# Kernel optimization log

Hardware: AMD Instinct MI355X
Metric: run time of the kernel (lower is better)

Reference implementation:

```python
import jax, jax.numpy as jnp
import numpy as np

B, I, O, N = 65536, 256, 32, 8


def chebyshev_basis(x, n):
    """Chebyshev polynomials T_0..T_{n-1} of x. x: [B, I] -> [B, I, n]."""
    T = [jnp.ones_like(x), x]
    for _ in range(n - 2):
        T.append(2.0 * x * T[-1] - T[-2])
    return jnp.stack(T[:n], axis=-1)


def setup_inputs() -> dict:
    key = jax.random.key(0)
    k1, k2 = jax.random.split(key)
    # inputs live on [-1, 1], the natural Chebyshev domain
    x = jax.random.uniform(k1, (B, I), jnp.float32, minval=-1.0, maxval=1.0)
    # weight init mirrors torch: uniform(-weight_magnitude/in, weight_magnitude/in)
    w = jax.random.uniform(k2, (O, I, N), jnp.float32, minval=-1.0 / I, maxval=1.0 / I)
    return {"x": x, "w": w}


def reference(x, w):
    n = w.shape[-1]
    phi = chebyshev_basis(x, n)          # [B, I, n] basis expansion
    out = jnp.einsum("bin,oin->bo", phi, w)  # weighted contraction
    return out
```

## Files before the change

### kernel.cpp

```cpp
#include <hip/hip_runtime.h>
#include <hip/hip_bf16.h>


typedef __attribute__((ext_vector_type(8)))  short bf16x8;
typedef __attribute__((ext_vector_type(16))) float f32x16;
typedef __attribute__((ext_vector_type(4)))  float f32x4;

__device__ __forceinline__ short f2b(float f) {
    __hip_bfloat16 h = __float2bfloat16(f);
    short s;
    __builtin_memcpy(&s, &h, sizeof(s));
    return s;
}

__device__ __forceinline__ unsigned pkbf_tr(float lo, float hi) {
    unsigned a, b;
    __builtin_memcpy(&a, &hi, 4);
    __builtin_memcpy(&b, &lo, 4);
    return __builtin_amdgcn_perm(a, b, 0x07060302u);
}

__global__ __launch_bounds__(256) void prep_w_kernel(const float* __restrict__ w,
                                                     short* __restrict__ wB) {
    int idx = blockIdx.x * 256 + threadIdx.x;
    int kc2 = idx >> 9;
    int l   = (idx >> 3) & 63;
    int jj  = idx & 7;
    int jjp = (jj >= 2 && jj < 6) ? (jj ^ 6) : jj;
    int o = l & 31, g = l >> 5;
    int i = 2 * kc2 + (jjp >> 2);
    int n = 4 * g + (jjp & 3);
    wB[idx] = f2b(w[(o * 256 + i) * 8 + n]);
}

__global__ __launch_bounds__(256, 4) void cheb_mm_kernel(const float* __restrict__ x,
                                                         const short* __restrict__ wB,
                                                         float* __restrict__ out) {
    __shared__ float smem[8192];
    const int tid = threadIdx.x;
    const int wv  = tid >> 6;
    const int l   = tid & 63;
    const int g   = l >> 5;
    const int r0  = l & 31;
    const long long rowB = (long long)blockIdx.x * 32;

    const bf16x8* wq = (const bf16x8*)wB + wv * 2048 + l;
    bf16x8 bfc[8];
    #pragma unroll
    for (int p = 0; p < 8; ++p) bfc[p] = wq[p * 64];

    {
        const float4* xg4 = (const float4*)(x + rowB * 256);
        const int f4l = l & 15;
        const int rsub = l >> 4;
        float4 stg[8];
        #pragma unroll
        for (int q = 0; q < 8; ++q)
            stg[q] = xg4[(q * 4 + rsub) * 64 + wv * 16 + f4l];
        #pragma unroll
        for (int q = 0; q < 8; ++q) {
            const int row  = q * 4 + rsub;
            const int base = row * 256 + wv * 64;
            const int s    = row & 31;
            const int p0 = 2 * f4l, p1 = 2 * f4l + 1;
            *(float2*)&smem[base + 2 * (p0 ^ s)] = make_float2(stg[q].x, stg[q].y);
            *(float2*)&smem[base + 2 * (p1 ^ s)] = make_float2(stg[q].z, stg[q].w);
        }
    }

    f32x16 accA{}, accB{};
    const float* sf = smem;
    const int base0 = r0 * 256 + wv * 64 + g + (r0 << 1);

    float xc[4];
    #pragma unroll
    for (int j = 0; j < 4; ++j) xc[j] = sf[base0 ^ (j << 1)];

    #pragma unroll
    for (int t = 0; t < 32; ++t) {
        const bf16x8 bfrag = bfc[t & 7];
        const float  xv    = xc[t & 3];
        if (t + 8 < 32) bfc[t & 7] = wq[(t + 8) * 64];
        if (t + 4 < 32) xc[t & 3]  = sf[base0 ^ ((t + 4) << 1)];

        const float x2 = xv + xv;
        const float T2 = fmaf(x2, xv, -1.f);
        const float T3 = fmaf(x2, T2, -xv);
        const float T4 = fmaf(x2, T3, -T2);
        const float T5 = fmaf(x2, T4, -T3);
        const float T6 = fmaf(x2, T5, -T4);
        const float T7 = fmaf(x2, T6, -T5);
        unsigned R0 = pkbf_tr(1.f, xv);
        unsigned R1 = pkbf_tr(T2, T3);
        unsigned R2 = pkbf_tr(T4, T5);
        unsigned R3 = pkbf_tr(T6, T7);
        auto r02 = __builtin_amdgcn_permlane32_swap(R0, R2, false, false);
        auto r13 = __builtin_amdgcn_permlane32_swap(R1, R3, false, false);
        union { unsigned u[4]; bf16x8 v; } af;
        af.u[0] = r02[0]; af.u[1] = r02[1];
        af.u[2] = r13[0]; af.u[3] = r13[1];
        if (t & 1)
            accB = __builtin_amdgcn_mfma_f32_32x32x16_bf16(af.v, bfrag, accB, 0, 0, 0);
        else
            accA = __builtin_amdgcn_mfma_f32_32x32x16_bf16(af.v, bfrag, accA, 0, 0, 0);
    }
    const f32x16 acc = accA + accB;

    #pragma unroll
    for (int r = 0; r < 16; ++r) {
        const int rloc = (r & 3) + 8 * (r >> 2) + 4 * g;
        smem[rloc * 256 + wv * 64 + r0] = acc[r];
    }
    __syncthreads();

    {
        float* op = out + rowB * 32;
        const int f   = tid * 4;
        const int row = f >> 5;
        const int c2  = f & 31;
        const int b   = row * 256 + c2;
        f32x4 v0 = *(const f32x4*)&smem[b];
        f32x4 v1 = *(const f32x4*)&smem[b + 64];
        f32x4 v2 = *(const f32x4*)&smem[b + 128];
        f32x4 v3 = *(const f32x4*)&smem[b + 192];
        f32x4 s = (v0 + v1) + (v2 + v3);
        *(f32x4*)(op + f) = s;
    }
}

extern "C" void kernel_launch(void* const* d_in, const int* in_sizes, int n_in,
                              void* d_out, int out_size, void* d_ws, size_t ws_size,
                              hipStream_t stream) {
    const float* x = (const float*)d_in[0];
    const float* w = (const float*)d_in[1];
    float* out = (float*)d_out;
    short* wB = (short*)d_ws;

    prep_w_kernel<<<256, 256, 0, stream>>>(w, wB);
    cheb_mm_kernel<<<2048, 256, 0, stream>>>(x, wB, out);
}
```

Before: 28.95 us.

## Transpose per-wave x tile in LDS and split staging into two halves

```diff
diff --git a/kernel.cpp b/kernel.cpp
--- a/kernel.cpp
+++ b/kernel.cpp
@@ -33,7 +33,7 @@
     wB[idx] = f2b(w[(o * 256 + i) * 8 + n]);
 }
 
-__global__ __launch_bounds__(256, 4) void cheb_mm_kernel(const float* __restrict__ x,
+__global__ __launch_bounds__(256, 3) void cheb_mm_kernel(const float* __restrict__ x,
                                                          const short* __restrict__ wB,
                                                          float* __restrict__ out) {
     __shared__ float smem[8192];
@@ -42,87 +42,134 @@
     const int l   = tid & 63;
     const int g   = l >> 5;
     const int r0  = l & 31;
+    const int wvS = wv * 2048;
     const long long rowB = (long long)blockIdx.x * 32;
 
-    const bf16x8* wq = (const bf16x8*)wB + wv * 2048 + l;
+    const float4* xg4 = (const float4*)(x + rowB * 256);
+    const bf16x8* wq  = (const bf16x8*)wB + wv * 2048 + l;
+
+    const int srow8 = l >> 3;
+    const int sf4   = l & 7;
+
+    float4 s0[4], s1[4];
+    #pragma unroll
+    for (int q = 0; q < 4; ++q)
+        s0[q] = xg4[(q * 8 + srow8) * 64 + wv * 16 + sf4];
+    #pragma unroll
+    for (int q = 0; q < 4; ++q)
+        s1[q] = xg4[(q * 8 + srow8) * 64 + wv * 16 + 8 + sf4];
     bf16x8 bfc[8];
     #pragma unroll
     for (int p = 0; p < 8; ++p) bfc[p] = wq[p * 64];
 
-    {
-        const float4* xg4 = (const float4*)(x + rowB * 256);
-        const int f4l = l & 15;
-        const int rsub = l >> 4;
-        float4 stg[8];
-        #pragma unroll
-        for (int q = 0; q < 8; ++q)
-            stg[q] = xg4[(q * 4 + rsub) * 64 + wv * 16 + f4l];
-        #pragma unroll
-        for (int q = 0; q < 8; ++q) {
-            const int row  = q * 4 + rsub;
-            const int base = row * 256 + wv * 64;
-            const int s    = row & 31;
-            const int p0 = 2 * f4l, p1 = 2 * f4l + 1;
-            *(float2*)&smem[base + 2 * (p0 ^ s)] = make_float2(stg[q].x, stg[q].y);
-            *(float2*)&smem[base + 2 * (p1 ^ s)] = make_float2(stg[q].z, stg[q].w);
-        }
+    #pragma unroll
+    for (int q = 0; q < 4; ++q) {
+        const int row = q * 8 + srow8;
+        const int kf0 = 4 * sf4;
+        smem[wvS + (kf0 + 0) * 32 + row] = s0[q].x;
+        smem[wvS + (kf0 + 1) * 32 + row] = s0[q].y;
+        smem[wvS + (kf0 + 2) * 32 + row] = s0[q].z;
+        smem[wvS + (kf0 + 3) * 32 + row] = s0[q].w;
     }
 
     f32x16 accA{}, accB{};
     const float* sf = smem;
-    const int base0 = r0 * 256 + wv * 64 + g + (r0 << 1);
+    const int base0 = wvS + g * 32 + r0;
 
-    float xc[4];
-    #pragma unroll
-    for (int j = 0; j < 4; ++j) xc[j] = sf[base0 ^ (j << 1)];
+    {
+        float xc[4];
+        #pragma unroll
+        for (int j = 0; j < 4; ++j) xc[j] = sf[base0 + j * 64];
+        #pragma unroll
+        for (int t = 0; t < 16; ++t) {
+            const bf16x8 bfrag = bfc[t & 7];
+            const float  xv    = xc[t & 3];
+            bfc[t & 7] = wq[(t + 8) * 64];
+            if (t + 4 < 16) xc[t & 3] = sf[base0 + (t + 4) * 64];
+
+            const float x2 = xv + xv;
+            const float T2 = fmaf(x2, xv, -1.f);
+            const float T3 = fmaf(x2, T2, -xv);
+            const float T4 = fmaf(x2, T3, -T2);
+            const float T5 = fmaf(x2, T4, -T3);
+            const float T6 = fmaf(x2, T5, -T4);
+            const float T7 = fmaf(x2, T6, -T5);
+            unsigned R0 = pkbf_tr(1.f, xv);
+            unsigned R1 = pkbf_tr(T2, T3);
+            unsigned R2 = pkbf_tr(T4, T5);
+            unsigned R3 = pkbf_tr(T6, T7);
+            auto r02 = __builtin_amdgcn_permlane32_swap(R0, R2, false, false);
+            auto r13 = __builtin_amdgcn_permlane32_swap(R1, R3, false, false);
+            union { unsigned u[4]; bf16x8 v; } af;
+            af.u[0] = r02[0]; af.u[1] = r02[1];
+            af.u[2] = r13[0]; af.u[3] = r13[1];
+            if (t & 1)
+                accB = __builtin_amdgcn_mfma_f32_32x32x16_bf16(af.v, bfrag, accB, 0, 0, 0);
+            else
+                accA = __builtin_amdgcn_mfma_f32_32x32x16_bf16(af.v, bfrag, accA, 0, 0, 0);
+        }
+    }
 
     #pragma unroll
-    for (int t = 0; t < 32; ++t) {
-        const bf16x8 bfrag = bfc[t & 7];
-        const float  xv    = xc[t & 3];
-        if (t + 8 < 32) bfc[t & 7] = wq[(t + 8) * 64];
-        if (t + 4 < 32) xc[t & 3]  = sf[base0 ^ ((t + 4) << 1)];
+    for (int q = 0; q < 4; ++q) {
+        const int row = q * 8 + srow8;
+        const int kf0 = 32 + 4 * sf4;
+        smem[wvS + (kf0 + 0) * 32 + row] = s1[q].x;
+        smem[wvS + (kf0 + 1) * 32 + row] = s1[q].y;
+        smem[wvS + (kf0 + 2) * 32 + row] = s1[q].z;
+        smem[wvS + (kf0 + 3) * 32 + row] = s1[q].w;
+    }
 
-        const float x2 = xv + xv;
-        const float T2 = fmaf(x2, xv, -1.f);
-        const float T3 = fmaf(x2, T2, -xv);
-        const float T4 = fmaf(x2, T3, -T2);
-        const float T5 = fmaf(x2, T4, -T3);
-        const float T6 = fmaf(x2, T5, -T4);
-        const float T7 = fmaf(x2, T6, -T5);
-        unsigned R0 = pkbf_tr(1.f, xv);
-        unsigned R1 = pkbf_tr(T2, T3);
-        unsigned R2 = pkbf_tr(T4, T5);
-        unsigned R3 = pkbf_tr(T6, T7);
-        auto r02 = __builtin_amdgcn_permlane32_swap(R0, R2, false, false);
-        auto r13 = __builtin_amdgcn_permlane32_swap(R1, R3, false, false);
-        union { unsigned u[4]; bf16x8 v; } af;
-        af.u[0] = r02[0]; af.u[1] = r02[1];
-        af.u[2] = r13[0]; af.u[3] = r13[1];
-        if (t & 1)
-            accB = __builtin_amdgcn_mfma_f32_32x32x16_bf16(af.v, bfrag, accB, 0, 0, 0);
-        else
-            accA = __builtin_amdgcn_mfma_f32_32x32x16_bf16(af.v, bfrag, accA, 0, 0, 0);
+    {
+        float xc[4];
+        #pragma unroll
+        for (int j = 0; j < 4; ++j) xc[j] = sf[base0 + (16 + j) * 64];
+        #pragma unroll
+        for (int j = 0; j < 16; ++j) {
+            const int t = 16 + j;
+            const bf16x8 bfrag = bfc[t & 7];
+            const float  xv    = xc[j & 3];
+            if (t + 8 < 32) bfc[t & 7] = wq[(t + 8) * 64];
+            if (j + 4 < 16) xc[j & 3] = sf[base0 + (t + 4) * 64];
+
+            const float x2 = xv + xv;
+            const float T2 = fmaf(x2, xv, -1.f);
+            const float T3 = fmaf(x2, T2, -xv);
+            const float T4 = fmaf(x2, T3, -T2);
+            const float T5 = fmaf(x2, T4, -T3);
+            const float T6 = fmaf(x2, T5, -T4);
+            const float T7 = fmaf(x2, T6, -T5);
+            unsigned R0 = pkbf_tr(1.f, xv);
+            unsigned R1 = pkbf_tr(T2, T3);
+            unsigned R2 = pkbf_tr(T4, T5);
+            unsigned R3 = pkbf_tr(T6, T7);
+            auto r02 = __builtin_amdgcn_permlane32_swap(R0, R2, false, false);
+            auto r13 = __builtin_amdgcn_permlane32_swap(R1, R3, false, false);
+            union { unsigned u[4]; bf16x8 v; } af;
+            af.u[0] = r02[0]; af.u[1] = r02[1];
+            af.u[2] = r13[0]; af.u[3] = r13[1];
+            if (t & 1)
+                accB = __builtin_amdgcn_mfma_f32_32x32x16_bf16(af.v, bfrag, accB, 0, 0, 0);
+            else
+                accA = __builtin_amdgcn_mfma_f32_32x32x16_bf16(af.v, bfrag, accA, 0, 0, 0);
+        }
     }
     const f32x16 acc = accA + accB;
 
     #pragma unroll
     for (int r = 0; r < 16; ++r) {
         const int rloc = (r & 3) + 8 * (r >> 2) + 4 * g;
-        smem[rloc * 256 + wv * 64 + r0] = acc[r];
+        smem[wvS + rloc * 32 + r0] = acc[r];
     }
     __syncthreads();
 
     {
         float* op = out + rowB * 32;
-        const int f   = tid * 4;
-        const int row = f >> 5;
-        const int c2  = f & 31;
-        const int b   = row * 256 + c2;
-        f32x4 v0 = *(const f32x4*)&smem[b];
-        f32x4 v1 = *(const f32x4*)&smem[b + 64];
-        f32x4 v2 = *(const f32x4*)&smem[b + 128];
-        f32x4 v3 = *(const f32x4*)&smem[b + 192];
+        const int f = tid * 4;
+        f32x4 v0 = *(const f32x4*)&smem[f];
+        f32x4 v1 = *(const f32x4*)&smem[2048 + f];
+        f32x4 v2 = *(const f32x4*)&smem[4096 + f];
+        f32x4 v3 = *(const f32x4*)&smem[6144 + f];
         f32x4 s = (v0 + v1) + (v2 + v3);
         *(f32x4*)(op + f) = s;
     }
```

Result: no change. 28.54 us (-1.4%).
